# Optimization experiments

Measured on AMD Instinct MI355X. Metric: run time of the kernel, lower is better.

## Reference

```python
import jax, jax.numpy as jnp
import numpy as np

NUM_HEADS = 16

def setup_inputs() -> dict:
    key = jax.random.key(0)
    ks = jax.random.split(key, 9)
    B, S, D = 2, 2048, 1024
    scale = 1.0 / np.sqrt(D)
    x = jax.random.normal(ks[0], (B, S, D), dtype=jnp.float32)
    def lin(k):
        kw, kb = jax.random.split(k)
        w = jax.random.uniform(kw, (D, D), jnp.float32, -scale, scale)
        b = jax.random.uniform(kb, (D,), jnp.float32, -scale, scale)
        return w, b
    wq, bq = lin(ks[1])
    wk, bk = lin(ks[2])
    wv, bv = lin(ks[3])
    wo, bo = lin(ks[4])
    return {"x": x, "wq": wq, "bq": bq, "wk": wk, "bk": bk,
            "wv": wv, "bv": bv, "wo": wo, "bo": bo}

def reference(x, wq, bq, wk, bk, wv, bv, wo, bo):
    # Prefill path: past_kv=None, use_cache=False, dropout in eval mode (identity).
    B, S, D = x.shape
    H = NUM_HEADS
    Hd = D // H
    # Linear layers: y = x @ W^T + b (torch nn.Linear convention)
    q = (x @ wq.T + bq).reshape(B, S, H, Hd)
    k = (x @ wk.T + bk).reshape(B, S, H, Hd)
    v = (x @ wv.T + bv).reshape(B, S, H, Hd)
    # scores: (B, H, S, S)
    scores = jnp.einsum("bqhd,bkhd->bhqk", q, k) / np.sqrt(Hd).astype(np.float32)
    # causal mask (seq_len > 1 and past_kv is None)
    causal = jnp.tril(jnp.ones((S, S), dtype=bool))
    scores = jnp.where(causal, scores, -jnp.inf)
    probs = jax.nn.softmax(scores, axis=-1)
    attn = jnp.einsum("bhqk,bkhd->bqhd", probs, v).reshape(B, S, D)
    return attn @ wo.T + bo
```

## Files before the change

kernel.cpp:

```cpp
#include <hip/hip_runtime.h>
#include <hip/hip_bf16.h>
#include <math.h>

constexpr int Bt   = 2;
constexpr int Sseq = 2048;
constexpr int Dm   = 1024;
constexpr int Hh   = 16;
constexpr int Mrows = Bt * Sseq;
constexpr int Kd    = 1024;

typedef __attribute__((ext_vector_type(8)))  short bf16x8;
typedef __attribute__((ext_vector_type(4)))  float f32x4;
typedef __attribute__((ext_vector_type(16))) float f32x16;

__device__ __forceinline__ ushort bfhi(float x) {
    __hip_bfloat16 h = __float2bfloat16(x);
    return *reinterpret_cast<ushort*>(&h);
}
__device__ __forceinline__ float bf2f(ushort u) {
    __hip_bfloat16 h;
    *reinterpret_cast<ushort*>(&h) = u;
    return __bfloat162float(h);
}
__device__ __forceinline__ void split2(float x, ushort& h, ushort& l) {
    h = bfhi(x);
    l = bfhi(x - bf2f(h));
}

template<int MODE>
__global__ __launch_bounds__(256)
void gemm_bf16x2(const float* __restrict__ A,
                 const float* __restrict__ W0, const float* __restrict__ W1,
                 const float* __restrict__ W2,
                 const float* __restrict__ b0, const float* __restrict__ b1,
                 const float* __restrict__ b2,
                 float* __restrict__ Cf,
                 ushort* __restrict__ qk_hi, ushort* __restrict__ qk_lo,
                 ushort* __restrict__ vt_hi, ushort* __restrict__ vt_lo)
{
    __shared__ alignas(16) ushort As[128 * 64];
    __shared__ alignas(16) ushort Bs[128 * 64];

    const int tid = threadIdx.x, lane = tid & 63, w = tid >> 6;

    const int gx = gridDim.x;
    int bid = blockIdx.y * gx + blockIdx.x;
    int cpx = (gx * gridDim.y) >> 3;
    int sb  = (bid & 7) * cpx + (bid >> 3);
    const int m0 = (sb / gx) * 128;
    const int j0 = (sb % gx) * 128;

    const int wsel = j0 >> 10;
    const float* __restrict__ W    = (wsel == 0) ? W0 : ((wsel == 1) ? W1 : W2);
    const float* __restrict__ bias = (wsel == 0) ? b0 : ((wsel == 1) ? b1 : b2);
    const int jj0 = j0 & 1023;

    const int wr = w >> 1, wc = w & 1;
    const int rl = lane & 15, kq = lane >> 4;
    const int sw0 = rl & 7;

    const int srow  = tid >> 1;
    const int khalf = tid & 1;
    const int rsw   = srow & 7;

    const float* ga0 = A + (size_t)(m0  + srow) * Kd + khalf * 16;
    const float* gb0 = W + (size_t)(jj0 + srow) * Kd + khalf * 16;

    f32x4 acc[4][4] = {};
    float av[16], bv[16];

    #pragma unroll
    for (int p = 0; p < 4; ++p) {
        *(float4*)&av[p * 4] = *(const float4*)(ga0 + p * 4);
        *(float4*)&bv[p * 4] = *(const float4*)(gb0 + p * 4);
    }

    for (int k0 = 0; k0 < Kd; k0 += 32) {
        __syncthreads();
        {
            ushort* pa = As + srow * 64;
            ushort* pb = Bs + srow * 64;
            #pragma unroll
            for (int t = 0; t < 2; ++t) {
                bf16x8 hia, loa, hib, lob;
                #pragma unroll
                for (int e = 0; e < 8; ++e) {
                    float xa = av[t * 8 + e], xb = bv[t * 8 + e];
                    ushort ha, la, hb, lb;
                    split2(xa, ha, la); split2(xb, hb, lb);
                    hia[e] = (short)ha; loa[e] = (short)la;
                    hib[e] = (short)hb; lob[e] = (short)lb;
                }
                int s = khalf * 2 + t;
                *(bf16x8*)(pa + ((s    ) ^ rsw) * 8) = hia;
                *(bf16x8*)(pa + ((s + 4) ^ rsw) * 8) = loa;
                *(bf16x8*)(pb + ((s    ) ^ rsw) * 8) = hib;
                *(bf16x8*)(pb + ((s + 4) ^ rsw) * 8) = lob;
            }
        }
        __syncthreads();

        if (k0 + 32 < Kd) {
            #pragma unroll
            for (int p = 0; p < 4; ++p) {
                *(float4*)&av[p * 4] = *(const float4*)(ga0 + k0 + 32 + p * 4);
                *(float4*)&bv[p * 4] = *(const float4*)(gb0 + k0 + 32 + p * 4);
            }
        }

        bf16x8 ah[4], al[4], bh[4], bl[4];
        #pragma unroll
        for (int i = 0; i < 4; ++i) {
            const ushort* pa = As + (wr * 64 + i * 16 + rl) * 64;
            ah[i] = *(const bf16x8*)(pa + ((kq    ) ^ sw0) * 8);
            al[i] = *(const bf16x8*)(pa + ((kq + 4) ^ sw0) * 8);
            const ushort* pb = Bs + (wc * 64 + i * 16 + rl) * 64;
            bh[i] = *(const bf16x8*)(pb + ((kq    ) ^ sw0) * 8);
            bl[i] = *(const bf16x8*)(pb + ((kq + 4) ^ sw0) * 8);
        }
        __builtin_amdgcn_s_setprio(1);
        #pragma unroll
        for (int i = 0; i < 4; ++i)
            #pragma unroll
            for (int j = 0; j < 4; ++j) {
                acc[i][j] = __builtin_amdgcn_mfma_f32_16x16x32_bf16(ah[i], bh[j], acc[i][j], 0, 0, 0);
                acc[i][j] = __builtin_amdgcn_mfma_f32_16x16x32_bf16(ah[i], bl[j], acc[i][j], 0, 0, 0);
                acc[i][j] = __builtin_amdgcn_mfma_f32_16x16x32_bf16(al[i], bh[j], acc[i][j], 0, 0, 0);
            }
        __builtin_amdgcn_s_setprio(0);
    }

    #pragma unroll
    for (int i = 0; i < 4; ++i)
        #pragma unroll
        for (int j = 0; j < 4; ++j) {
            int col = j0 + wc * 64 + j * 16 + rl;
            float bv_ = bias[col & 1023];
            int token0 = m0 + wr * 64 + i * 16 + kq * 4;
            if constexpr (MODE == 1) {
                #pragma unroll
                for (int r = 0; r < 4; ++r)
                    Cf[(size_t)(token0 + r) * 1024 + col] = acc[i][j][r] + bv_;
            } else {
                if (col < 2048) {
                    float scale = (col < 1024) ? 0.125f : 1.0f;
                    #pragma unroll
                    for (int r = 0; r < 4; ++r) {
                        float val = (acc[i][j][r] + bv_) * scale;
                        ushort hs, ls;
                        split2(val, hs, ls);
                        size_t idx = (size_t)(token0 + r) * 2048 + col;
                        qk_hi[idx] = hs;
                        qk_lo[idx] = ls;
                    }
                } else {
                    int cc = col - 2048;
                    int hh = cc >> 6, dd = cc & 63;
                    int bb = token0 >> 11, s0 = token0 & 2047;
                    ushort hs[4], ls[4];
                    #pragma unroll
                    for (int r = 0; r < 4; ++r)
                        split2(acc[i][j][r] + bv_, hs[r], ls[r]);
                    size_t vrow = ((size_t)(bb * 16 + hh) * 64 + dd) * 2048 + s0;
                    *(ushort4*)(vt_hi + vrow) = make_ushort4(hs[0], hs[1], hs[2], hs[3]);
                    *(ushort4*)(vt_lo + vrow) = make_ushort4(ls[0], ls[1], ls[2], ls[3]);
                }
            }
        }
}

__global__ __launch_bounds__(256)
void attn_mfma32(const ushort* __restrict__ qk_hi, const ushort* __restrict__ qk_lo,
                 const ushort* __restrict__ vt_hi, const ushort* __restrict__ vt_lo,
                 float* __restrict__ aout)
{
    __shared__ alignas(16) ushort Kh[4096], Kl[4096], Vh[4096], Vl[4096];

    const int xx = blockIdx.x;
    const int qt = (xx & 1) ? (xx >> 1) : (15 - (xx >> 1));
    const int h  = blockIdx.y, b = blockIdx.z;
    const int q0 = qt * 128;
    const int tid = threadIdx.x, l = tid & 63, w = tid >> 6;
    const int lo5 = l & 31, hi = l >> 5;

    bf16x8 qh[4], ql[4];
    {
        const size_t qrow = (size_t)(b * Sseq + q0 + w * 32 + lo5);
        #pragma unroll
        for (int s = 0; s < 4; ++s) {
            size_t g = qrow * 2048 + h * 64 + s * 16 + hi * 8;
            qh[s] = *(const bf16x8*)(qk_hi + g);
            ql[s] = *(const bf16x8*)(qk_lo + g);
        }
    }

    f32x16 accO[2] = {};
    float m_r = -INFINITY, l_r = 0.0f;
    const int qg = q0 + w * 32 + lo5;

    const int srow = tid >> 2, sc2 = tid & 3;
    const size_t kbase = (size_t)(b * Sseq) * 2048 + 1024 + h * 64 + sc2 * 16;
    const size_t vbase = ((size_t)((b * 16 + h) * 64) + srow) * 2048 + sc2 * 16;
    const int swA = (sc2 * 2 + 0) ^ (srow & 7);
    const int swB = (sc2 * 2 + 1) ^ (srow & 7);

    bf16x8 stg[8];
    auto ISSUE = [&](int kv0) {
        size_t gk = kbase + (size_t)(kv0 + srow) * 2048;
        size_t gv = vbase + kv0;
        stg[0] = *(const bf16x8*)(qk_hi + gk);
        stg[1] = *(const bf16x8*)(qk_hi + gk + 8);
        stg[2] = *(const bf16x8*)(qk_lo + gk);
        stg[3] = *(const bf16x8*)(qk_lo + gk + 8);
        stg[4] = *(const bf16x8*)(vt_hi + gv);
        stg[5] = *(const bf16x8*)(vt_hi + gv + 8);
        stg[6] = *(const bf16x8*)(vt_lo + gv);
        stg[7] = *(const bf16x8*)(vt_lo + gv + 8);
    };

    const int NT = 2 * qt + 2;
    ISSUE(0);

    for (int kt = 0; kt < NT; ++kt) {
        __syncthreads();
        {
            *(bf16x8*)(Kh + srow * 64 + swA * 8) = stg[0];
            *(bf16x8*)(Kh + srow * 64 + swB * 8) = stg[1];
            *(bf16x8*)(Kl + srow * 64 + swA * 8) = stg[2];
            *(bf16x8*)(Kl + srow * 64 + swB * 8) = stg[3];
            *(bf16x8*)(Vh + srow * 64 + swA * 8) = stg[4];
            *(bf16x8*)(Vh + srow * 64 + swB * 8) = stg[5];
            *(bf16x8*)(Vl + srow * 64 + swA * 8) = stg[6];
            *(bf16x8*)(Vl + srow * 64 + swB * 8) = stg[7];
        }
        __syncthreads();

        if (kt + 1 < NT) ISSUE((kt + 1) * 64);

        const int kv0 = kt * 64;

        f32x16 sc[2] = {};
        #pragma unroll
        for (int s = 0; s < 4; ++s) {
            __builtin_amdgcn_s_setprio(1);
            #pragma unroll
            for (int n = 0; n < 2; ++n) {
                int row = n * 32 + lo5;
                int sl = (s * 2 + hi) ^ (row & 7);
                bf16x8 kh = *(const bf16x8*)(Kh + row * 64 + sl * 8);
                bf16x8 kl = *(const bf16x8*)(Kl + row * 64 + sl * 8);
                sc[n] = __builtin_amdgcn_mfma_f32_32x32x16_bf16(kh, qh[s], sc[n], 0, 0, 0);
                sc[n] = __builtin_amdgcn_mfma_f32_32x32x16_bf16(kh, ql[s], sc[n], 0, 0, 0);
                sc[n] = __builtin_amdgcn_mfma_f32_32x32x16_bf16(kl, qh[s], sc[n], 0, 0, 0);
            }
            __builtin_amdgcn_s_setprio(0);
        }

        if (kt >= 2 * qt) {
            #pragma unroll
            for (int n = 0; n < 2; ++n)
                #pragma unroll
                for (int r = 0; r < 16; ++r) {
                    int kv = kv0 + n * 32 + ((r & 3) + 8 * (r >> 2) + 4 * hi);
                    if (kv > qg) sc[n][r] = -INFINITY;
                }
        }

        float vmax = -INFINITY;
        #pragma unroll
        for (int n = 0; n < 2; ++n)
            #pragma unroll
            for (int r = 0; r < 16; ++r)
                vmax = fmaxf(vmax, sc[n][r]);
        vmax = fmaxf(vmax, __shfl_xor(vmax, 32));
        float mnew = fmaxf(m_r, vmax);
        float fs = __expf(m_r - mnew);
        m_r = mnew;

        uint phk[2][8], plk[2][8];
        float sum = 0.0f;
        #pragma unroll
        for (int n = 0; n < 2; ++n)
            #pragma unroll
            for (int j = 0; j < 8; ++j) {
                float p0 = __expf(sc[n][2 * j]     - mnew);
                float p1 = __expf(sc[n][2 * j + 1] - mnew);
                sum += p0 + p1;
                ushort h0, l0, h1, l1;
                split2(p0, h0, l0);
                split2(p1, h1, l1);
                phk[n][j] = (uint)h0 | ((uint)h1 << 16);
                plk[n][j] = (uint)l0 | ((uint)l1 << 16);
            }
        sum += __shfl_xor(sum, 32);
        l_r = l_r * fs + sum;

        #pragma unroll
        for (int nd = 0; nd < 2; ++nd)
            #pragma unroll
            for (int r = 0; r < 16; ++r)
                accO[nd][r] *= fs;

        #pragma unroll
        for (int step = 0; step < 4; ++step) {
            const int n  = step >> 1;
            const int io = (step & 1) * 4 + hi * 2;
            const int is = (step & 1) * 4 + (1 - hi) * 2;
            uint oh0 = phk[n][io], oh1 = phk[n][io + 1];
            uint ol0 = plk[n][io], ol1 = plk[n][io + 1];
            uint sh0 = (uint)__shfl_xor((int)phk[n][is],     32);
            uint sh1 = (uint)__shfl_xor((int)phk[n][is + 1], 32);
            uint sl0 = (uint)__shfl_xor((int)plk[n][is],     32);
            uint sl1 = (uint)__shfl_xor((int)plk[n][is + 1], 32);
            uint fh[4], fl[4];
            if (hi) { fh[0] = sh0; fh[1] = sh1; fh[2] = oh0; fh[3] = oh1;
                      fl[0] = sl0; fl[1] = sl1; fl[2] = ol0; fl[3] = ol1; }
            else    { fh[0] = oh0; fh[1] = oh1; fh[2] = sh0; fh[3] = sh1;
                      fl[0] = ol0; fl[1] = ol1; fl[2] = sl0; fl[3] = sl1; }
            bf16x8 ph = *reinterpret_cast<bf16x8*>(fh);
            bf16x8 pl = *reinterpret_cast<bf16x8*>(fl);

            __builtin_amdgcn_s_setprio(1);
            #pragma unroll
            for (int nd = 0; nd < 2; ++nd) {
                int row = nd * 32 + lo5;
                int sl_ = (step * 2 + hi) ^ (row & 7);
                bf16x8 vh = *(const bf16x8*)(Vh + row * 64 + sl_ * 8);
                bf16x8 vl = *(const bf16x8*)(Vl + row * 64 + sl_ * 8);
                accO[nd] = __builtin_amdgcn_mfma_f32_32x32x16_bf16(vh, ph, accO[nd], 0, 0, 0);
                accO[nd] = __builtin_amdgcn_mfma_f32_32x32x16_bf16(vh, pl, accO[nd], 0, 0, 0);
                accO[nd] = __builtin_amdgcn_mfma_f32_32x32x16_bf16(vl, ph, accO[nd], 0, 0, 0);
            }
            __builtin_amdgcn_s_setprio(0);
        }
    }

    {
        float inv = 1.0f / l_r;
        const size_t token = (size_t)(b * Sseq + q0 + w * 32 + lo5);
        #pragma unroll
        for (int nd = 0; nd < 2; ++nd)
            #pragma unroll
            for (int rg = 0; rg < 4; ++rg) {
                float4 o = { accO[nd][4 * rg + 0] * inv, accO[nd][4 * rg + 1] * inv,
                             accO[nd][4 * rg + 2] * inv, accO[nd][4 * rg + 3] * inv };
                *(float4*)&aout[token * 1024 + h * 64 + nd * 32 + 8 * rg + 4 * hi] = o;
            }
    }
}

extern "C" void kernel_launch(void* const* d_in, const int* in_sizes, int n_in,
                              void* d_out, int out_size, void* d_ws, size_t ws_size,
                              hipStream_t stream)
{
    const float* x  = (const float*)d_in[0];
    const float* wq = (const float*)d_in[1];
    const float* bq = (const float*)d_in[2];
    const float* wk = (const float*)d_in[3];
    const float* bk = (const float*)d_in[4];
    const float* wv = (const float*)d_in[5];
    const float* bv = (const float*)d_in[6];
    const float* wo = (const float*)d_in[7];
    const float* bo = (const float*)d_in[8];
    float* out = (float*)d_out;

    const size_t NEED = 67108864;
    if (ws_size < NEED) return;

    char* p = (char*)d_ws;
    ushort* qk_hi = (ushort*)(p);
    ushort* qk_lo = (ushort*)(p + 16777216);
    ushort* vt_hi = (ushort*)(p + 33554432);
    ushort* vt_lo = (ushort*)(p + 41943040);
    float*  attn  = (float*) (p + 50331648);

    gemm_bf16x2<0><<<dim3(24, 32), 256, 0, stream>>>(
        x, wq, wk, wv, bq, bk, bv, nullptr, qk_hi, qk_lo, vt_hi, vt_lo);

    attn_mfma32<<<dim3(16, Hh, Bt), 256, 0, stream>>>(
        qk_hi, qk_lo, vt_hi, vt_lo, attn);

    gemm_bf16x2<1><<<dim3(8, 32), 256, 0, stream>>>(
        attn, wo, wo, wo, bo, bo, bo, out, nullptr, nullptr, nullptr, nullptr);
}
```

Baseline: 429.5 us.

## Pre-split inputs into bf16 hi/lo planes and shrink attention tiles to 64 queries

```diff
diff --git a/kernel.cpp b/kernel.cpp
--- a/kernel.cpp
+++ b/kernel.cpp
@@ -9,6 +9,8 @@
 constexpr int Mrows = Bt * Sseq;
 constexpr int Kd    = 1024;
 
+constexpr float QSCALE = 0.18033688011112042f;
+
 typedef __attribute__((ext_vector_type(8)))  short bf16x8;
 typedef __attribute__((ext_vector_type(4)))  float f32x4;
 typedef __attribute__((ext_vector_type(16))) float f32x16;
@@ -27,109 +29,31 @@
     l = bfhi(x - bf2f(h));
 }
 
+__global__ __launch_bounds__(256)
+void split_fp32(const float* __restrict__ in, ushort* __restrict__ hi,
+                ushort* __restrict__ lo, int n4)
+{
+    int i = blockIdx.x * blockDim.x + threadIdx.x;
+    int stride = gridDim.x * blockDim.x;
+    for (; i < n4; i += stride) {
+        float4 v = ((const float4*)in)[i];
+        float vv[4] = {v.x, v.y, v.z, v.w};
+        ushort hs[4], ls[4];
+        #pragma unroll
+        for (int j = 0; j < 4; ++j) split2(vv[j], hs[j], ls[j]);
+        *(ushort4*)&hi[i * 4] = make_ushort4(hs[0], hs[1], hs[2], hs[3]);
+        *(ushort4*)&lo[i * 4] = make_ushort4(ls[0], ls[1], ls[2], ls[3]);
+    }
+}
+
 template<int MODE>
-__global__ __launch_bounds__(256)
-void gemm_bf16x2(const float* __restrict__ A,
-                 const float* __restrict__ W0, const float* __restrict__ W1,
-                 const float* __restrict__ W2,
-                 const float* __restrict__ b0, const float* __restrict__ b1,
-                 const float* __restrict__ b2,
-                 float* __restrict__ Cf,
-                 ushort* __restrict__ qk_hi, ushort* __restrict__ qk_lo,
-                 ushort* __restrict__ vt_hi, ushort* __restrict__ vt_lo)
+__device__ __forceinline__ void gemm_epilogue(
+    f32x4 (&acc)[4][4], int m0, int j0, int wr, int wc, int rl, int kq,
+    const float* b0, const float* b1, const float* b2,
+    float* Cf, ushort* qk_hi, ushort* qk_lo, ushort* vt_hi, ushort* vt_lo)
 {
-    __shared__ alignas(16) ushort As[128 * 64];
-    __shared__ alignas(16) ushort Bs[128 * 64];
-
-    const int tid = threadIdx.x, lane = tid & 63, w = tid >> 6;
-
-    const int gx = gridDim.x;
-    int bid = blockIdx.y * gx + blockIdx.x;
-    int cpx = (gx * gridDim.y) >> 3;
-    int sb  = (bid & 7) * cpx + (bid >> 3);
-    const int m0 = (sb / gx) * 128;
-    const int j0 = (sb % gx) * 128;
-
     const int wsel = j0 >> 10;
-    const float* __restrict__ W    = (wsel == 0) ? W0 : ((wsel == 1) ? W1 : W2);
-    const float* __restrict__ bias = (wsel == 0) ? b0 : ((wsel == 1) ? b1 : b2);
-    const int jj0 = j0 & 1023;
-
-    const int wr = w >> 1, wc = w & 1;
-    const int rl = lane & 15, kq = lane >> 4;
-    const int sw0 = rl & 7;
-
-    const int srow  = tid >> 1;
-    const int khalf = tid & 1;
-    const int rsw   = srow & 7;
-
-    const float* ga0 = A + (size_t)(m0  + srow) * Kd + khalf * 16;
-    const float* gb0 = W + (size_t)(jj0 + srow) * Kd + khalf * 16;
-
-    f32x4 acc[4][4] = {};
-    float av[16], bv[16];
-
-    #pragma unroll
-    for (int p = 0; p < 4; ++p) {
-        *(float4*)&av[p * 4] = *(const float4*)(ga0 + p * 4);
-        *(float4*)&bv[p * 4] = *(const float4*)(gb0 + p * 4);
-    }
-
-    for (int k0 = 0; k0 < Kd; k0 += 32) {
-        __syncthreads();
-        {
-            ushort* pa = As + srow * 64;
-            ushort* pb = Bs + srow * 64;
-            #pragma unroll
-            for (int t = 0; t < 2; ++t) {
-                bf16x8 hia, loa, hib, lob;
-                #pragma unroll
-                for (int e = 0; e < 8; ++e) {
-                    float xa = av[t * 8 + e], xb = bv[t * 8 + e];
-                    ushort ha, la, hb, lb;
-                    split2(xa, ha, la); split2(xb, hb, lb);
-                    hia[e] = (short)ha; loa[e] = (short)la;
-                    hib[e] = (short)hb; lob[e] = (short)lb;
-                }
-                int s = khalf * 2 + t;
-                *(bf16x8*)(pa + ((s    ) ^ rsw) * 8) = hia;
-                *(bf16x8*)(pa + ((s + 4) ^ rsw) * 8) = loa;
-                *(bf16x8*)(pb + ((s    ) ^ rsw) * 8) = hib;
-                *(bf16x8*)(pb + ((s + 4) ^ rsw) * 8) = lob;
-            }
-        }
-        __syncthreads();
-
-        if (k0 + 32 < Kd) {
-            #pragma unroll
-            for (int p = 0; p < 4; ++p) {
-                *(float4*)&av[p * 4] = *(const float4*)(ga0 + k0 + 32 + p * 4);
-                *(float4*)&bv[p * 4] = *(const float4*)(gb0 + k0 + 32 + p * 4);
-            }
-        }
-
-        bf16x8 ah[4], al[4], bh[4], bl[4];
-        #pragma unroll
-        for (int i = 0; i < 4; ++i) {
-            const ushort* pa = As + (wr * 64 + i * 16 + rl) * 64;
-            ah[i] = *(const bf16x8*)(pa + ((kq    ) ^ sw0) * 8);
-            al[i] = *(const bf16x8*)(pa + ((kq + 4) ^ sw0) * 8);
-            const ushort* pb = Bs + (wc * 64 + i * 16 + rl) * 64;
-            bh[i] = *(const bf16x8*)(pb + ((kq    ) ^ sw0) * 8);
-            bl[i] = *(const bf16x8*)(pb + ((kq + 4) ^ sw0) * 8);
-        }
-        __builtin_amdgcn_s_setprio(1);
-        #pragma unroll
-        for (int i = 0; i < 4; ++i)
-            #pragma unroll
-            for (int j = 0; j < 4; ++j) {
-                acc[i][j] = __builtin_amdgcn_mfma_f32_16x16x32_bf16(ah[i], bh[j], acc[i][j], 0, 0, 0);
-                acc[i][j] = __builtin_amdgcn_mfma_f32_16x16x32_bf16(ah[i], bl[j], acc[i][j], 0, 0, 0);
-                acc[i][j] = __builtin_amdgcn_mfma_f32_16x16x32_bf16(al[i], bh[j], acc[i][j], 0, 0, 0);
-            }
-        __builtin_amdgcn_s_setprio(0);
-    }
-
+    const float* bias = (wsel == 0) ? b0 : ((wsel == 1) ? b1 : b2);
     #pragma unroll
     for (int i = 0; i < 4; ++i)
         #pragma unroll
@@ -143,7 +67,7 @@
                     Cf[(size_t)(token0 + r) * 1024 + col] = acc[i][j][r] + bv_;
             } else {
                 if (col < 2048) {
-                    float scale = (col < 1024) ? 0.125f : 1.0f;
+                    float scale = (col < 1024) ? QSCALE : 1.0f;
                     #pragma unroll
                     for (int r = 0; r < 4; ++r) {
                         float val = (acc[i][j][r] + bv_) * scale;
@@ -169,17 +93,218 @@
         }
 }
 
+template<int MODE>
 __global__ __launch_bounds__(256)
-void attn_mfma32(const ushort* __restrict__ qk_hi, const ushort* __restrict__ qk_lo,
-                 const ushort* __restrict__ vt_hi, const ushort* __restrict__ vt_lo,
-                 float* __restrict__ aout)
+void gemm_planes(const ushort* __restrict__ Ah, const ushort* __restrict__ Al,
+                 const ushort* __restrict__ Wh, const ushort* __restrict__ Wl,
+                 const float* __restrict__ b0, const float* __restrict__ b1,
+                 const float* __restrict__ b2,
+                 float* __restrict__ Cf,
+                 ushort* __restrict__ qk_hi, ushort* __restrict__ qk_lo,
+                 ushort* __restrict__ vt_hi, ushort* __restrict__ vt_lo)
+{
+    __shared__ alignas(16) ushort As[128 * 64];
+    __shared__ alignas(16) ushort Bs[128 * 64];
+
+    const int tid = threadIdx.x, lane = tid & 63, w = tid >> 6;
+
+    const int gx = gridDim.x;
+    int bid = blockIdx.y * gx + blockIdx.x;
+    int cpx = (gx * gridDim.y) >> 3;
+    int sb  = (bid & 7) * cpx + (bid >> 3);
+    const int m0 = (sb / gx) * 128;
+    const int j0 = (sb % gx) * 128;
+
+    const int wr = w >> 1, wc = w & 1;
+    const int rl = lane & 15, kq = lane >> 4;
+    const int sw0 = rl & 7;
+
+    const int srow  = tid >> 1;
+    const int khalf = tid & 1;
+    const int rsw   = srow & 7;
+
+    const ushort* ga_h = Ah + (size_t)(m0 + srow) * Kd + khalf * 16;
+    const ushort* ga_l = Al + (size_t)(m0 + srow) * Kd + khalf * 16;
+    const ushort* gb_h = Wh + (size_t)(j0 + srow) * Kd + khalf * 16;
+    const ushort* gb_l = Wl + (size_t)(j0 + srow) * Kd + khalf * 16;
+
+    f32x4 acc[4][4] = {};
+    bf16x8 sA[4], sB[4];
+
+    auto LOAD = [&](int k0) {
+        sA[0] = *(const bf16x8*)(ga_h + k0);
+        sA[1] = *(const bf16x8*)(ga_h + k0 + 8);
+        sA[2] = *(const bf16x8*)(ga_l + k0);
+        sA[3] = *(const bf16x8*)(ga_l + k0 + 8);
+        sB[0] = *(const bf16x8*)(gb_h + k0);
+        sB[1] = *(const bf16x8*)(gb_h + k0 + 8);
+        sB[2] = *(const bf16x8*)(gb_l + k0);
+        sB[3] = *(const bf16x8*)(gb_l + k0 + 8);
+    };
+
+    LOAD(0);
+    for (int k0 = 0; k0 < Kd; k0 += 32) {
+        __syncthreads();
+        {
+            ushort* pa = As + srow * 64;
+            ushort* pb = Bs + srow * 64;
+            #pragma unroll
+            for (int t = 0; t < 2; ++t) {
+                int s = khalf * 2 + t;
+                *(bf16x8*)(pa + ((s    ) ^ rsw) * 8) = sA[t];
+                *(bf16x8*)(pa + ((s + 4) ^ rsw) * 8) = sA[t + 2];
+                *(bf16x8*)(pb + ((s    ) ^ rsw) * 8) = sB[t];
+                *(bf16x8*)(pb + ((s + 4) ^ rsw) * 8) = sB[t + 2];
+            }
+        }
+        __syncthreads();
+
+        if (k0 + 32 < Kd) LOAD(k0 + 32);
+
+        bf16x8 ah[4], al[4], bh[4], bl[4];
+        #pragma unroll
+        for (int i = 0; i < 4; ++i) {
+            const ushort* pa = As + (wr * 64 + i * 16 + rl) * 64;
+            ah[i] = *(const bf16x8*)(pa + ((kq    ) ^ sw0) * 8);
+            al[i] = *(const bf16x8*)(pa + ((kq + 4) ^ sw0) * 8);
+            const ushort* pb = Bs + (wc * 64 + i * 16 + rl) * 64;
+            bh[i] = *(const bf16x8*)(pb + ((kq    ) ^ sw0) * 8);
+            bl[i] = *(const bf16x8*)(pb + ((kq + 4) ^ sw0) * 8);
+        }
+        __builtin_amdgcn_s_setprio(1);
+        #pragma unroll
+        for (int i = 0; i < 4; ++i)
+            #pragma unroll
+            for (int j = 0; j < 4; ++j) {
+                acc[i][j] = __builtin_amdgcn_mfma_f32_16x16x32_bf16(ah[i], bh[j], acc[i][j], 0, 0, 0);
+                acc[i][j] = __builtin_amdgcn_mfma_f32_16x16x32_bf16(ah[i], bl[j], acc[i][j], 0, 0, 0);
+                acc[i][j] = __builtin_amdgcn_mfma_f32_16x16x32_bf16(al[i], bh[j], acc[i][j], 0, 0, 0);
+            }
+        __builtin_amdgcn_s_setprio(0);
+    }
+
+    gemm_epilogue<MODE>(acc, m0, j0, wr, wc, rl, kq, b0, b1, b2,
+                        Cf, qk_hi, qk_lo, vt_hi, vt_lo);
+}
+
+template<int MODE>
+__global__ __launch_bounds__(256)
+void gemm_bf16x2(const float* __restrict__ A,
+                 const float* __restrict__ W0, const float* __restrict__ W1,
+                 const float* __restrict__ W2,
+                 const float* __restrict__ b0, const float* __restrict__ b1,
+                 const float* __restrict__ b2,
+                 float* __restrict__ Cf,
+                 ushort* __restrict__ qk_hi, ushort* __restrict__ qk_lo,
+                 ushort* __restrict__ vt_hi, ushort* __restrict__ vt_lo)
+{
+    __shared__ alignas(16) ushort As[128 * 64];
+    __shared__ alignas(16) ushort Bs[128 * 64];
+
+    const int tid = threadIdx.x, lane = tid & 63, w = tid >> 6;
+
+    const int gx = gridDim.x;
+    int bid = blockIdx.y * gx + blockIdx.x;
+    int cpx = (gx * gridDim.y) >> 3;
+    int sb  = (bid & 7) * cpx + (bid >> 3);
+    const int m0 = (sb / gx) * 128;
+    const int j0 = (sb % gx) * 128;
+
+    const int wsel = j0 >> 10;
+    const float* __restrict__ W = (wsel == 0) ? W0 : ((wsel == 1) ? W1 : W2);
+    const int jj0 = j0 & 1023;
+
+    const int wr = w >> 1, wc = w & 1;
+    const int rl = lane & 15, kq = lane >> 4;
+    const int sw0 = rl & 7;
+
+    const int srow  = tid >> 1;
+    const int khalf = tid & 1;
+    const int rsw   = srow & 7;
+
+    const float* ga0 = A + (size_t)(m0  + srow) * Kd + khalf * 16;
+    const float* gb0 = W + (size_t)(jj0 + srow) * Kd + khalf * 16;
+
+    f32x4 acc[4][4] = {};
+    float av[16], bv[16];
+
+    #pragma unroll
+    for (int p = 0; p < 4; ++p) {
+        *(float4*)&av[p * 4] = *(const float4*)(ga0 + p * 4);
+        *(float4*)&bv[p * 4] = *(const float4*)(gb0 + p * 4);
+    }
+
+    for (int k0 = 0; k0 < Kd; k0 += 32) {
+        __syncthreads();
+        {
+            ushort* pa = As + srow * 64;
+            ushort* pb = Bs + srow * 64;
+            #pragma unroll
+            for (int t = 0; t < 2; ++t) {
+                bf16x8 hia, loa, hib, lob;
+                #pragma unroll
+                for (int e = 0; e < 8; ++e) {
+                    float xa = av[t * 8 + e], xb = bv[t * 8 + e];
+                    ushort ha, la, hb, lb;
+                    split2(xa, ha, la); split2(xb, hb, lb);
+                    hia[e] = (short)ha; loa[e] = (short)la;
+                    hib[e] = (short)hb; lob[e] = (short)lb;
+                }
+                int s = khalf * 2 + t;
+                *(bf16x8*)(pa + ((s    ) ^ rsw) * 8) = hia;
+                *(bf16x8*)(pa + ((s + 4) ^ rsw) * 8) = loa;
+                *(bf16x8*)(pb + ((s    ) ^ rsw) * 8) = hib;
+                *(bf16x8*)(pb + ((s + 4) ^ rsw) * 8) = lob;
+            }
+        }
+        __syncthreads();
+
+        if (k0 + 32 < Kd) {
+            #pragma unroll
+            for (int p = 0; p < 4; ++p) {
+                *(float4*)&av[p * 4] = *(const float4*)(ga0 + k0 + 32 + p * 4);
+                *(float4*)&bv[p * 4] = *(const float4*)(gb0 + k0 + 32 + p * 4);
+            }
+        }
+
+        bf16x8 ah[4], al[4], bh[4], bl[4];
+        #pragma unroll
+        for (int i = 0; i < 4; ++i) {
+            const ushort* pa = As + (wr * 64 + i * 16 + rl) * 64;
+            ah[i] = *(const bf16x8*)(pa + ((kq    ) ^ sw0) * 8);
+            al[i] = *(const bf16x8*)(pa + ((kq + 4) ^ sw0) * 8);
+            const ushort* pb = Bs + (wc * 64 + i * 16 + rl) * 64;
+            bh[i] = *(const bf16x8*)(pb + ((kq    ) ^ sw0) * 8);
+            bl[i] = *(const bf16x8*)(pb + ((kq + 4) ^ sw0) * 8);
+        }
+        __builtin_amdgcn_s_setprio(1);
+        #pragma unroll
+        for (int i = 0; i < 4; ++i)
+            #pragma unroll
+            for (int j = 0; j < 4; ++j) {
+                acc[i][j] = __builtin_amdgcn_mfma_f32_16x16x32_bf16(ah[i], bh[j], acc[i][j], 0, 0, 0);
+                acc[i][j] = __builtin_amdgcn_mfma_f32_16x16x32_bf16(ah[i], bl[j], acc[i][j], 0, 0, 0);
+                acc[i][j] = __builtin_amdgcn_mfma_f32_16x16x32_bf16(al[i], bh[j], acc[i][j], 0, 0, 0);
+            }
+        __builtin_amdgcn_s_setprio(0);
+    }
+
+    gemm_epilogue<MODE>(acc, m0, j0, wr, wc, rl, kq, b0, b1, b2,
+                        Cf, qk_hi, qk_lo, vt_hi, vt_lo);
+}
+
+template<bool WSPLIT>
+__global__ __launch_bounds__(128)
+void attn64(const ushort* __restrict__ qk_hi, const ushort* __restrict__ qk_lo,
+            const ushort* __restrict__ vt_hi, const ushort* __restrict__ vt_lo,
+            float* __restrict__ outF, ushort* __restrict__ oHi, ushort* __restrict__ oLo)
 {
     __shared__ alignas(16) ushort Kh[4096], Kl[4096], Vh[4096], Vl[4096];
 
     const int xx = blockIdx.x;
-    const int qt = (xx & 1) ? (xx >> 1) : (15 - (xx >> 1));
+    const int qt = (xx & 1) ? (xx >> 1) : (31 - (xx >> 1));
     const int h  = blockIdx.y, b = blockIdx.z;
-    const int q0 = qt * 128;
+    const int q0 = qt * 64;
     const int tid = threadIdx.x, l = tid & 63, w = tid >> 6;
     const int lo5 = l & 31, hi = l >> 5;
 
@@ -198,40 +323,35 @@
     float m_r = -INFINITY, l_r = 0.0f;
     const int qg = q0 + w * 32 + lo5;
 
-    const int srow = tid >> 2, sc2 = tid & 3;
-    const size_t kbase = (size_t)(b * Sseq) * 2048 + 1024 + h * 64 + sc2 * 16;
-    const size_t vbase = ((size_t)((b * 16 + h) * 64) + srow) * 2048 + sc2 * 16;
-    const int swA = (sc2 * 2 + 0) ^ (srow & 7);
-    const int swB = (sc2 * 2 + 1) ^ (srow & 7);
-
-    bf16x8 stg[8];
+    const int srow = tid >> 1, sh = tid & 1;
+    const size_t kbase = (size_t)(b * Sseq) * 2048 + 1024 + h * 64 + sh * 32;
+    const size_t vbase = ((size_t)((b * 16 + h) * 64) + srow) * 2048 + sh * 32;
+
+    bf16x8 sKh[4], sKl[4], sVh[4], sVl[4];
     auto ISSUE = [&](int kv0) {
         size_t gk = kbase + (size_t)(kv0 + srow) * 2048;
         size_t gv = vbase + kv0;
-        stg[0] = *(const bf16x8*)(qk_hi + gk);
-        stg[1] = *(const bf16x8*)(qk_hi + gk + 8);
-        stg[2] = *(const bf16x8*)(qk_lo + gk);
-        stg[3] = *(const bf16x8*)(qk_lo + gk + 8);
-        stg[4] = *(const bf16x8*)(vt_hi + gv);
-        stg[5] = *(const bf16x8*)(vt_hi + gv + 8);
-        stg[6] = *(const bf16x8*)(vt_lo + gv);
-        stg[7] = *(const bf16x8*)(vt_lo + gv + 8);
+        #pragma unroll
+        for (int t = 0; t < 4; ++t) {
+            sKh[t] = *(const bf16x8*)(qk_hi + gk + t * 8);
+            sKl[t] = *(const bf16x8*)(qk_lo + gk + t * 8);
+            sVh[t] = *(const bf16x8*)(vt_hi + gv + t * 8);
+            sVl[t] = *(const bf16x8*)(vt_lo + gv + t * 8);
+        }
     };
 
-    const int NT = 2 * qt + 2;
+    const int NT = qt + 1;
     ISSUE(0);
 
     for (int kt = 0; kt < NT; ++kt) {
         __syncthreads();
-        {
-            *(bf16x8*)(Kh + srow * 64 + swA * 8) = stg[0];
-            *(bf16x8*)(Kh + srow * 64 + swB * 8) = stg[1];
-            *(bf16x8*)(Kl + srow * 64 + swA * 8) = stg[2];
-            *(bf16x8*)(Kl + srow * 64 + swB * 8) = stg[3];
-            *(bf16x8*)(Vh + srow * 64 + swA * 8) = stg[4];
-            *(bf16x8*)(Vh + srow * 64 + swB * 8) = stg[5];
-            *(bf16x8*)(Vl + srow * 64 + swA * 8) = stg[6];
-            *(bf16x8*)(Vl + srow * 64 + swB * 8) = stg[7];
+        #pragma unroll
+        for (int t = 0; t < 4; ++t) {
+            int sw = (((sh * 4 + t) ^ (srow & 7))) * 8;
+            *(bf16x8*)(Kh + srow * 64 + sw) = sKh[t];
+            *(bf16x8*)(Kl + srow * 64 + sw) = sKl[t];
+            *(bf16x8*)(Vh + srow * 64 + sw) = sVh[t];
+            *(bf16x8*)(Vl + srow * 64 + sw) = sVl[t];
         }
         __syncthreads();
 
@@ -256,7 +376,7 @@
             __builtin_amdgcn_s_setprio(0);
         }
 
-        if (kt >= 2 * qt) {
+        if (kt == qt) {
             #pragma unroll
             for (int n = 0; n < 2; ++n)
                 #pragma unroll
@@ -274,7 +394,7 @@
                 vmax = fmaxf(vmax, sc[n][r]);
         vmax = fmaxf(vmax, __shfl_xor(vmax, 32));
         float mnew = fmaxf(m_r, vmax);
-        float fs = __expf(m_r - mnew);
+        float fs = exp2f(m_r - mnew);
         m_r = mnew;
 
         uint phk[2][8], plk[2][8];
@@ -283,8 +403,8 @@
         for (int n = 0; n < 2; ++n)
             #pragma unroll
             for (int j = 0; j < 8; ++j) {
-                float p0 = __expf(sc[n][2 * j]     - mnew);
-                float p1 = __expf(sc[n][2 * j + 1] - mnew);
+                float p0 = exp2f(sc[n][2 * j]     - mnew);
+                float p1 = exp2f(sc[n][2 * j + 1] - mnew);
                 sum += p0 + p1;
                 ushort h0, l0, h1, l1;
                 split2(p0, h0, l0);
@@ -342,9 +462,19 @@
         for (int nd = 0; nd < 2; ++nd)
             #pragma unroll
             for (int rg = 0; rg < 4; ++rg) {
-                float4 o = { accO[nd][4 * rg + 0] * inv, accO[nd][4 * rg + 1] * inv,
-                             accO[nd][4 * rg + 2] * inv, accO[nd][4 * rg + 3] * inv };
-                *(float4*)&aout[token * 1024 + h * 64 + nd * 32 + 8 * rg + 4 * hi] = o;
+                size_t idx = token * 1024 + h * 64 + nd * 32 + 8 * rg + 4 * hi;
+                if constexpr (WSPLIT) {
+                    ushort hs[4], ls[4];
+                    #pragma unroll
+                    for (int e = 0; e < 4; ++e)
+                        split2(accO[nd][4 * rg + e] * inv, hs[e], ls[e]);
+                    *(ushort4*)&oHi[idx] = make_ushort4(hs[0], hs[1], hs[2], hs[3]);
+                    *(ushort4*)&oLo[idx] = make_ushort4(ls[0], ls[1], ls[2], ls[3]);
+                } else {
+                    float4 o = { accO[nd][4 * rg + 0] * inv, accO[nd][4 * rg + 1] * inv,
+                                 accO[nd][4 * rg + 2] * inv, accO[nd][4 * rg + 3] * inv };
+                    *(float4*)&outF[idx] = o;
+                }
             }
     }
 }
@@ -364,22 +494,52 @@
     const float* bo = (const float*)d_in[8];
     float* out = (float*)d_out;
 
-    const size_t NEED = 67108864;
-    if (ws_size < NEED) return;
+    const size_t NEED1 = 67108864;
+    const size_t NEED2 = 100663296;
+    if (ws_size < NEED1) return;
 
     char* p = (char*)d_ws;
     ushort* qk_hi = (ushort*)(p);
     ushort* qk_lo = (ushort*)(p + 16777216);
     ushort* vt_hi = (ushort*)(p + 33554432);
     ushort* vt_lo = (ushort*)(p + 41943040);
-    float*  attn  = (float*) (p + 50331648);
-
-    gemm_bf16x2<0><<<dim3(24, 32), 256, 0, stream>>>(
-        x, wq, wk, wv, bq, bk, bv, nullptr, qk_hi, qk_lo, vt_hi, vt_lo);
-
-    attn_mfma32<<<dim3(16, Hh, Bt), 256, 0, stream>>>(
-        qk_hi, qk_lo, vt_hi, vt_lo, attn);
-
-    gemm_bf16x2<1><<<dim3(8, 32), 256, 0, stream>>>(
-        attn, wo, wo, wo, bo, bo, bo, out, nullptr, nullptr, nullptr, nullptr);
-}
+
+    if (ws_size >= NEED2) {
+        ushort* at_hi = (ushort*)(p + 50331648);
+        ushort* at_lo = (ushort*)(p + 58720256);
+        ushort* xp_hi = (ushort*)(p + 67108864);
+        ushort* xp_lo = (ushort*)(p + 75497472);
+        ushort* w1_hi = (ushort*)(p + 83886080);
+        ushort* w1_lo = (ushort*)(p + 90177536);
+        ushort* w2_hi = (ushort*)(p + 96468992);
+        ushort* w2_lo = (ushort*)(p + 98566144);
+
+        split_fp32<<<1024, 256, 0, stream>>>(x,  xp_hi, xp_lo, 1048576);
+        split_fp32<<<512,  256, 0, stream>>>(wq, w1_hi,           w1_lo,           262144);
+        split_fp32<<<512,  256, 0, stream>>>(wk, w1_hi + 1048576, w1_lo + 1048576, 262144);
+        split_fp32<<<512,  256, 0, stream>>>(wv, w1_hi + 2097152, w1_lo + 2097152, 262144);
+        split_fp32<<<512,  256, 0, stream>>>(wo, w2_hi,           w2_lo,           262144);
+
+        gemm_planes<0><<<dim3(24, 32), 256, 0, stream>>>(
+            xp_hi, xp_lo, w1_hi, w1_lo, bq, bk, bv,
+            nullptr, qk_hi, qk_lo, vt_hi, vt_lo);
+
+        attn64<true><<<dim3(32, Hh, Bt), 128, 0, stream>>>(
+            qk_hi, qk_lo, vt_hi, vt_lo, nullptr, at_hi, at_lo);
+
+        gemm_planes<1><<<dim3(8, 32), 256, 0, stream>>>(
+            at_hi, at_lo, w2_hi, w2_lo, bo, bo, bo,
+            out, nullptr, nullptr, nullptr, nullptr);
+    } else {
+        float* attn = (float*)(p + 50331648);
+
+        gemm_bf16x2<0><<<dim3(24, 32), 256, 0, stream>>>(
+            x, wq, wk, wv, bq, bk, bv, nullptr, qk_hi, qk_lo, vt_hi, vt_lo);
+
+        attn64<false><<<dim3(32, Hh, Bt), 128, 0, stream>>>(
+            qk_hi, qk_lo, vt_hi, vt_lo, attn, nullptr, nullptr);
+
+        gemm_bf16x2<1><<<dim3(8, 32), 256, 0, stream>>>(
+            attn, wo, wo, wo, bo, bo, bo, out, nullptr, nullptr, nullptr, nullptr);
+    }
+}
```

New measurement: 505.7 us. +17.7%, slower.
